# Optimization experiments

Measured on AMD Instinct MI355X. Metric: run time of the kernel, lower is better.

## Reference

```python
import jax, jax.numpy as jnp
import numpy as np
import math
from itertools import permutations

B, C_IN, C_OUT, K, N, D, F_DIM = 2, 4, 8, 4, 224, 2, 128


def _make_perms(k):
    # [k!, k, k] permutation matrices, same ordering as itertools.permutations
    nP = math.factorial(k)
    perms = np.zeros((nP, k, k), dtype=np.float32)
    for c, p in enumerate(permutations(range(k))):
        perms[c, np.arange(k), np.array(p)] = 1.0
    return jnp.asarray(perms)


def setup_inputs() -> dict:
    key = jax.random.key(0)
    ks = jax.random.split(key, 6)
    graph = jax.random.normal(ks[0], (B, C_IN, N, N), jnp.float32)
    types = jax.random.normal(ks[1], (B, C_IN, N), jnp.float32)
    features = jax.random.normal(ks[2], (B, N, F_DIM), jnp.float32)
    # xavier-uniform-ish scales for the learned kernels
    k_struct = jax.random.normal(ks[3], (C_OUT, C_IN, K, K), jnp.float32) * 0.3
    k_row = jax.random.normal(ks[4], (C_OUT, C_IN, K), jnp.float32) * 0.5
    k_col = jax.random.normal(ks[5], (C_OUT, C_IN, K), jnp.float32) * 0.5
    return {"graph": graph, "types": types, "features": features,
            "k_struct": k_struct, "k_row": k_row, "k_col": k_col}


def _forward(graph, types, features, k_struct, k_row, k_col):
    Bn, C, Nn, _ = graph.shape
    k = k_struct.shape[-1]
    new_k = (k - 1) * D + 1
    nH = Nn - new_k + 1            # square graph -> nW == nH
    n_sub = nH * nH
    idx = jnp.arange(nH)[:, None] + jnp.arange(k) * D  # [nH, k] dilated window indices

    # --- _prepare: dilated subgraph extraction (vectorized gather) ---
    g = graph[:, :, idx, :]            # [B,C,nH,k,N]
    g = g[..., idx]                    # [B,C,nH,k,nH,k]
    sub = jnp.transpose(g, (0, 2, 4, 1, 3, 5)).reshape(Bn, n_sub, C, k, k)
    rt = jnp.transpose(types[:, :, idx], (0, 2, 1, 3))  # [B,nH,C,k]
    row_t = jnp.broadcast_to(rt[:, :, None], (Bn, nH, nH, C, k)).reshape(Bn, n_sub, C, k)
    col_t = jnp.broadcast_to(rt[:, None, :], (Bn, nH, nH, C, k)).reshape(Bn, n_sub, C, k)
    rf = features[:, idx, :].sum(axis=-2)              # [B,nH,F]
    feats = rf[:, :, None, :] + rf[:, None, :, :]      # row_features + col_features
    h_mean = feats.reshape(Bn, n_sub, -1).mean(axis=1)  # [B,F]

    # --- permuted kernels ---
    perms = _make_perms(k)                                  # [P,k,k]
    Kp = jnp.einsum('pau,oiuv,pbv->oipab', perms, k_struct, perms)  # P K P^T
    Rp = jnp.einsum('pau,oiu->oipa', perms, k_row)
    Cp = jnp.einsum('pau,oiu->oipa', perms, k_col)

    subf = sub.reshape(-1, C, k, k)   # [n,i,a,b], n = B*n_sub
    rtf = row_t.reshape(-1, C, k)
    ctf = col_t.reshape(-1, C, k)

    # ||X - Y||_F^2 = ||X||^2 + ||Y||^2 - 2<X,Y>, avoids the huge broadcasted diff
    def sq_dist(x2_ni, y2_opi, cross_nopi):
        return y2_opi[None] + x2_ni[:, None, None, :] - 2.0 * cross_nopi

    G2 = jnp.sum(subf * subf, axis=(-2, -1))                       # [n,i]
    K2 = jnp.transpose(jnp.sum(Kp * Kp, axis=(-2, -1)), (0, 2, 1))  # [o,p,i]
    struct = sq_dist(G2, K2, jnp.einsum('niab,oipab->nopi', subf, Kp))
    R2 = jnp.transpose(jnp.sum(Rp * Rp, axis=-1), (0, 2, 1))
    rsim = sq_dist(jnp.sum(rtf * rtf, axis=-1), R2, jnp.einsum('nia,oipa->nopi', rtf, Rp))
    C2 = jnp.transpose(jnp.sum(Cp * Cp, axis=-1), (0, 2, 1))
    csim = sq_dist(jnp.sum(ctf * ctf, axis=-1), C2, jnp.einsum('nia,oipa->nopi', ctf, Cp))

    total = struct + rsim + csim            # [n, o, P, i]
    # maxpool over P of (-total), negated back == min over permutations of total
    pooled = jnp.min(total, axis=2)         # [n, o, i]
    sims = jnp.transpose(pooled.reshape(Bn, n_sub, -1), (0, 2, 1))  # [B, o*i, n_sub]
    out_sim = (1.0 - jax.nn.softmax(sims, axis=-1)) / sims.shape[-1]
    return h_mean, out_sim


def reference(graph, types, features, k_struct, k_row, k_col):
    return _forward(graph, types, features, k_struct, k_row, k_col)
```

## Files before the change

### kernel.cpp

```cpp
#include <hip/hip_runtime.h>
#include <hip/hip_bf16.h>

#define B_    2
#define CIN   4
#define COUT  8
#define KK    4
#define DD    2
#define NN    224
#define FDIM  128
#define NH    218
#define NSUB  (NH*NH)
#define NPERM 24
#define NROWS (B_*COUT*CIN)
#define NSUB4 (NSUB/4)
#define CH4   512
#define MB    ((NSUB4 + CH4 - 1) / CH4)
#define OG    2
#define NCH2  ((NSUB + 511) / 512)
#define NW    4
#define NPART (NCH2*NW)
#define NEGBIG (-3.4e38f)

typedef float v2f __attribute__((ext_vector_type(2)));

__device__ static constexpr int PERM[NPERM][4] = {
  {0,1,2,3},{0,1,3,2},{0,2,1,3},{0,2,3,1},{0,3,1,2},{0,3,2,1},
  {1,0,2,3},{1,0,3,2},{1,2,0,3},{1,2,3,0},{1,3,0,2},{1,3,2,0},
  {2,0,1,3},{2,0,3,1},{2,1,0,3},{2,1,3,0},{2,3,0,1},{2,3,1,0},
  {3,0,1,2},{3,0,2,1},{3,1,0,2},{3,1,2,0},{3,2,0,1},{3,2,1,0}
};

__global__ __launch_bounds__(64) void hmean_kernel(const float* __restrict__ features,
                                                   float* __restrict__ out) {
  int bf = blockIdx.x;
  int b = bf / FDIM, f = bf - b * FDIM;
  int lane = threadIdx.x;
  const float* fb = features + (size_t)b * NN * FDIM + f;
  float acc = 0.f;
  for (int r = lane; r < NN; r += 64) {
    int w = 0;
#pragma unroll
    for (int a = 0; a < KK; ++a) {
      int i0 = r - a * DD;
      if (0 <= i0 && i0 < NH) w++;
    }
    acc += (float)w * fb[(size_t)r * FDIM];
  }
#pragma unroll
  for (int off = 32; off > 0; off >>= 1) acc += __shfl_down(acc, off, 64);
  if (lane == 0) out[bf] = acc * (2.0f / (float)NH);
}

__global__ __launch_bounds__(256) void sims_kernel(
    const float* __restrict__ graph, const float* __restrict__ types,
    const float* __restrict__ ksA, const float* __restrict__ krA,
    const float* __restrict__ kcA, float* __restrict__ simsOut,
    float* __restrict__ partial)
{
  __shared__ float ls[COUT * CIN * 16];
  __shared__ float lr[COUT * CIN * 4];
  __shared__ float lc[COUT * CIN * 4];
  __shared__ float lK2[COUT * CIN];
  int t = threadIdx.x;
  for (int i = t; i < COUT * CIN * 16; i += 256) ls[i] = ksA[i];
  for (int i = t; i < COUT * CIN * 4; i += 256) { lr[i] = krA[i]; lc[i] = kcA[i]; }
  __syncthreads();
  if (t < COUT * CIN) {
    float k2 = 0.f;
#pragma unroll
    for (int u = 0; u < 16; ++u) k2 += ls[t * 16 + u] * ls[t * 16 + u];
#pragma unroll
    for (int u = 0; u < 4; ++u) k2 += lr[t * 4 + u] * lr[t * 4 + u] + lc[t * 4 + u] * lc[t * 4 + u];
    lK2[t] = k2;
  }
  __syncthreads();

  int s0r = blockIdx.x * 512 + t;
  int s1r = s0r + 256;
  bool v0 = (s0r < NSUB), v1 = (s1r < NSUB);
  int s0 = v0 ? s0r : (NSUB - 1);
  int s1 = v1 ? s1r : (NSUB - 1);
  int yi  = blockIdx.y;
  int og  = yi >> 3;
  int bci = yi & 7;
  int b   = bci >> 2;
  int ci  = bci & 3;
  int ii0 = s0 / NH, jj0 = s0 - ii0 * NH;
  int ii1 = s1 / NH, jj1 = s1 - ii1 * NH;

  const float* gi = graph + ((size_t)b * CIN + ci) * NN * NN;
  const float* ti = types + ((size_t)b * CIN + ci) * NN;

  v2f subv[16], rtv[4], ctv[4];
  v2f G2 = 0.f, T2r = 0.f, T2c = 0.f;
#pragma unroll
  for (int a = 0; a < KK; ++a) {
    const float* r0 = gi + (size_t)(ii0 + a * DD) * NN + jj0;
    const float* r1 = gi + (size_t)(ii1 + a * DD) * NN + jj1;
#pragma unroll
    for (int bb = 0; bb < KK; ++bb) {
      v2f v; v.x = r0[bb * DD]; v.y = r1[bb * DD];
      subv[a * 4 + bb] = v;
      G2 += v * v;
    }
    v2f rv; rv.x = ti[ii0 + a * DD]; rv.y = ti[ii1 + a * DD];
    v2f cv; cv.x = ti[jj0 + a * DD]; cv.y = ti[jj1 + a * DD];
    rtv[a] = rv; ctv[a] = cv;
    T2r += rv * rv; T2c += cv * cv;
  }
  v2f base0 = G2 + T2r + T2c;

  int wave = t >> 6, lane = t & 63;

#pragma unroll 1
  for (int oo = 0; oo < COUT / OG; ++oo) {
    int o = og * (COUT / OG) + oo;
    int oc = o * CIN + ci;
    float kS[16], kR[4], kC[4];
    {
      const float4* pS4 = (const float4*)(ls + oc * 16);
#pragma unroll
      for (int u = 0; u < 4; ++u) {
        float4 q = pS4[u];
        kS[u*4+0] = q.x; kS[u*4+1] = q.y; kS[u*4+2] = q.z; kS[u*4+3] = q.w;
      }
      float4 qr = *(const float4*)(lr + oc * 4);
      kR[0] = qr.x; kR[1] = qr.y; kR[2] = qr.z; kR[3] = qr.w;
      float4 qc = *(const float4*)(lc + oc * 4);
      kC[0] = qc.x; kC[1] = qc.y; kC[2] = qc.z; kC[3] = qc.w;
    }

    v2f C1[16];
#pragma unroll
    for (int a = 0; a < 4; ++a)
#pragma unroll
      for (int ap = 0; ap < 4; ++ap)
        C1[a * 4 + ap] = subv[a * 4 + a] * kS[ap * 4 + ap]
                       + rtv[a] * kR[ap] + ctv[a] * kC[ap];

    v2f pair01[16], pair23[16];
#pragma unroll
    for (int x = 0; x < 4; ++x)
#pragma unroll
      for (int y = 0; y < 4; ++y) {
        if (x == y) continue;
        pair01[x * 4 + y] = C1[0 * 4 + x] + C1[1 * 4 + y]
                          + subv[0*4+1] * kS[x*4+y] + subv[1*4+0] * kS[y*4+x];
        pair23[x * 4 + y] = C1[2 * 4 + x] + C1[3 * 4 + y]
                          + subv[2*4+3] * kS[x*4+y] + subv[3*4+2] * kS[y*4+x];
      }

    v2f maxcr = NEGBIG;
#pragma unroll
    for (int p = 0; p < NPERM; ++p) {
      const int p0 = PERM[p][0], p1 = PERM[p][1], p2 = PERM[p][2], p3 = PERM[p][3];
      v2f cr = pair01[p0 * 4 + p1] + pair23[p2 * 4 + p3];
      cr += subv[0*4+2] * kS[p0*4+p2];
      cr += subv[2*4+0] * kS[p2*4+p0];
      cr += subv[0*4+3] * kS[p0*4+p3];
      cr += subv[3*4+0] * kS[p3*4+p0];
      cr += subv[1*4+2] * kS[p1*4+p2];
      cr += subv[2*4+1] * kS[p2*4+p1];
      cr += subv[1*4+3] * kS[p1*4+p3];
      cr += subv[3*4+1] * kS[p3*4+p1];
      maxcr = __builtin_elementwise_max(maxcr, cr);
    }
    v2f best = base0 + lK2[oc] - 2.0f * maxcr;

    int rowIdx = (b * COUT + o) * CIN + ci;
    size_t rowbase = (size_t)rowIdx * NSUB;
    if (v0) simsOut[rowbase + s0r] = best.x;
    if (v1) simsOut[rowbase + s1r] = best.y;

    float bm0 = v0 ? best.x : NEGBIG;
    float bm1 = v1 ? best.y : NEGBIG;
    float m = fmaxf(bm0, bm1);
#pragma unroll
    for (int off = 32; off > 0; off >>= 1) m = fmaxf(m, __shfl_down(m, off, 64));
    m = __shfl(m, 0, 64);
    float e = 0.f;
    if (v0) e += __expf(bm0 - m);
    if (v1) e += __expf(bm1 - m);
#pragma unroll
    for (int off = 32; off > 0; off >>= 1) e += __shfl_down(e, off, 64);
    if (lane == 0) {
      int idx = ((rowIdx * NCH2 + blockIdx.x) * NW + wave) * 2;
      partial[idx] = m; partial[idx + 1] = e;
    }
  }
}

__global__ __launch_bounds__(256) void softmax_final(float* __restrict__ sims,
                                                     const float* __restrict__ partial) {
  int blk = blockIdx.x;
  int row = blk / MB;
  int ch  = blk - row * MB;
  int t = threadIdx.x;

  const float* pp = partial + (size_t)row * NPART * 2;
  float m = NEGBIG, l = 0.f;
  for (int i = t; i < NPART; i += 256) {
    float mi = pp[2 * i], li = pp[2 * i + 1];
    float M = fmaxf(m, mi);
    l = l * __expf(m - M) + li * __expf(mi - M);
    m = M;
  }
  __shared__ float ms[256], lsv[256];
  ms[t] = m; lsv[t] = l;
  __syncthreads();
  for (int off = 128; off > 0; off >>= 1) {
    if (t < off) {
      float m2 = ms[t + off], l2 = lsv[t + off];
      float M = fmaxf(ms[t], m2);
      lsv[t] = lsv[t] * __expf(ms[t] - M) + l2 * __expf(m2 - M);
      ms[t] = M;
    }
    __syncthreads();
  }
  float M = ms[0], invS = 1.0f / lsv[0];

  int base4 = ch * CH4;
  int n4 = NSUB4 - base4; if (n4 > CH4) n4 = CH4;
  float4* rp = (float4*)(sims + (size_t)row * NSUB) + base4;
  const float scale = 1.0f / (float)NSUB;
  for (int i = t; i < n4; i += 256) {
    float4 v = rp[i];
    v.x = (1.0f - __expf(v.x - M) * invS) * scale;
    v.y = (1.0f - __expf(v.y - M) * invS) * scale;
    v.z = (1.0f - __expf(v.z - M) * invS) * scale;
    v.w = (1.0f - __expf(v.w - M) * invS) * scale;
    rp[i] = v;
  }
}

extern "C" void kernel_launch(void* const* d_in, const int* in_sizes, int n_in,
                              void* d_out, int out_size, void* d_ws, size_t ws_size,
                              hipStream_t stream) {
  const float* graph    = (const float*)d_in[0];
  const float* types    = (const float*)d_in[1];
  const float* features = (const float*)d_in[2];
  const float* ks       = (const float*)d_in[3];
  const float* kr       = (const float*)d_in[4];
  const float* kc       = (const float*)d_in[5];
  float* out  = (float*)d_out;
  float* sims = out + B_ * FDIM;

  float* partial = (float*)d_ws;

  hmean_kernel<<<B_ * FDIM, 64, 0, stream>>>(features, out);
  dim3 sgrid(NCH2, B_ * CIN * OG);
  sims_kernel<<<sgrid, 256, 0, stream>>>(graph, types, ks, kr, kc, sims, partial);
  softmax_final<<<NROWS * MB, 256, 0, stream>>>(sims, partial);
}
```

Baseline: 103.7 us.

## Split softmax statistics into separate pass and add occupancy hint to sims kernel

Moves the per-wave max/exp-sum reductions out of the sims kernel into a new softmax_partial kernel that rereads sims in 2048-element chunks. softmax_final now merges only MB partials per row with a single-wave shuffle instead of a 256-thread shared-memory tree over many partials. The sims kernel also gets a launch_bounds occupancy hint of 4. The intent is to lighten the compute-heavy sims kernel and shrink the final merge, at the cost of an extra kernel launch and one more full read pass over the sims buffer.

New measurement: 100.8 us. 1.03x faster.

```diff
diff --git a/kernel.cpp b/kernel.cpp
--- a/kernel.cpp
+++ b/kernel.cpp
@@ -17,8 +17,6 @@
 #define MB    ((NSUB4 + CH4 - 1) / CH4)
 #define OG    2
 #define NCH2  ((NSUB + 511) / 512)
-#define NW    4
-#define NPART (NCH2*NW)
 #define NEGBIG (-3.4e38f)
 
 typedef float v2f __attribute__((ext_vector_type(2)));
@@ -51,11 +49,10 @@
   if (lane == 0) out[bf] = acc * (2.0f / (float)NH);
 }
 
-__global__ __launch_bounds__(256) void sims_kernel(
+__global__ __launch_bounds__(256, 4) void sims_kernel(
     const float* __restrict__ graph, const float* __restrict__ types,
     const float* __restrict__ ksA, const float* __restrict__ krA,
-    const float* __restrict__ kcA, float* __restrict__ simsOut,
-    float* __restrict__ partial)
+    const float* __restrict__ kcA, float* __restrict__ simsOut)
 {
   __shared__ float ls[COUT * CIN * 16];
   __shared__ float lr[COUT * CIN * 4];
@@ -110,8 +107,6 @@
   }
   v2f base0 = G2 + T2r + T2c;
 
-  int wave = t >> 6, lane = t & 63;
-
 #pragma unroll 1
   for (int oo = 0; oo < COUT / OG; ++oo) {
     int o = og * (COUT / OG) + oo;
@@ -167,57 +162,72 @@
     }
     v2f best = base0 + lK2[oc] - 2.0f * maxcr;
 
-    int rowIdx = (b * COUT + o) * CIN + ci;
-    size_t rowbase = (size_t)rowIdx * NSUB;
+    size_t rowbase = (size_t)((b * COUT + o) * CIN + ci) * NSUB;
     if (v0) simsOut[rowbase + s0r] = best.x;
     if (v1) simsOut[rowbase + s1r] = best.y;
-
-    float bm0 = v0 ? best.x : NEGBIG;
-    float bm1 = v1 ? best.y : NEGBIG;
-    float m = fmaxf(bm0, bm1);
-#pragma unroll
-    for (int off = 32; off > 0; off >>= 1) m = fmaxf(m, __shfl_down(m, off, 64));
-    m = __shfl(m, 0, 64);
-    float e = 0.f;
-    if (v0) e += __expf(bm0 - m);
-    if (v1) e += __expf(bm1 - m);
-#pragma unroll
-    for (int off = 32; off > 0; off >>= 1) e += __shfl_down(e, off, 64);
-    if (lane == 0) {
-      int idx = ((rowIdx * NCH2 + blockIdx.x) * NW + wave) * 2;
-      partial[idx] = m; partial[idx + 1] = e;
-    }
+  }
+}
+
+__global__ __launch_bounds__(256) void softmax_partial(const float* __restrict__ sims,
+                                                       float* __restrict__ partial) {
+  int ch = blockIdx.x, row = blockIdx.y;
+  int base4 = ch * CH4;
+  int n4 = NSUB4 - base4; if (n4 > CH4) n4 = CH4;
+  const float4* rp = (const float4*)(sims + (size_t)row * NSUB) + base4;
+  int t = threadIdx.x;
+  int wave = t >> 6, lane = t & 63;
+
+  float4 a0, a1;
+  bool h0 = (t < n4), h1 = (t + 256 < n4);
+  if (h0) a0 = rp[t];
+  if (h1) a1 = rp[t + 256];
+
+  float m = NEGBIG;
+  if (h0) m = fmaxf(fmaxf(a0.x, a0.y), fmaxf(a0.z, a0.w));
+  if (h1) m = fmaxf(m, fmaxf(fmaxf(a1.x, a1.y), fmaxf(a1.z, a1.w)));
+#pragma unroll
+  for (int off = 32; off > 0; off >>= 1) m = fmaxf(m, __shfl_down(m, off, 64));
+  __shared__ float red[8];
+  if (lane == 0) red[wave] = m;
+  __syncthreads();
+  float M = fmaxf(fmaxf(red[0], red[1]), fmaxf(red[2], red[3]));
+
+  float e = 0.f;
+  if (h0) e  = __expf(a0.x - M) + __expf(a0.y - M) + __expf(a0.z - M) + __expf(a0.w - M);
+  if (h1) e += __expf(a1.x - M) + __expf(a1.y - M) + __expf(a1.z - M) + __expf(a1.w - M);
+#pragma unroll
+  for (int off = 32; off > 0; off >>= 1) e += __shfl_down(e, off, 64);
+  if (lane == 0) red[4 + wave] = e;
+  __syncthreads();
+  if (t == 0) {
+    int idx = (row * MB + ch) * 2;
+    partial[idx] = M;
+    partial[idx + 1] = red[4] + red[5] + red[6] + red[7];
   }
 }
 
 __global__ __launch_bounds__(256) void softmax_final(float* __restrict__ sims,
                                                      const float* __restrict__ partial) {
-  int blk = blockIdx.x;
-  int row = blk / MB;
-  int ch  = blk - row * MB;
+  int ch = blockIdx.x, row = blockIdx.y;
   int t = threadIdx.x;
 
-  const float* pp = partial + (size_t)row * NPART * 2;
-  float m = NEGBIG, l = 0.f;
-  for (int i = t; i < NPART; i += 256) {
-    float mi = pp[2 * i], li = pp[2 * i + 1];
-    float M = fmaxf(m, mi);
-    l = l * __expf(m - M) + li * __expf(mi - M);
-    m = M;
-  }
-  __shared__ float ms[256], lsv[256];
-  ms[t] = m; lsv[t] = l;
-  __syncthreads();
-  for (int off = 128; off > 0; off >>= 1) {
-    if (t < off) {
-      float m2 = ms[t + off], l2 = lsv[t + off];
-      float M = fmaxf(ms[t], m2);
-      lsv[t] = lsv[t] * __expf(ms[t] - M) + l2 * __expf(m2 - M);
-      ms[t] = M;
-    }
-    __syncthreads();
-  }
-  float M = ms[0], invS = 1.0f / lsv[0];
+  __shared__ float sM, sInv;
+  if (t < 64) {
+    const float* pp = partial + row * MB * 2;
+    float m = NEGBIG, l = 0.f;
+    if (t < MB) { m = pp[2 * t]; l = pp[2 * t + 1]; }
+#pragma unroll
+    for (int off = 32; off > 0; off >>= 1) {
+      float m2 = __shfl_down(m, off, 64);
+      float l2 = __shfl_down(l, off, 64);
+      float M = fmaxf(m, m2);
+      l = l * __expf(m - M) + l2 * __expf(m2 - M);
+      m = M;
+    }
+    if (t == 0) { sM = m; sInv = 1.0f / l; }
+  }
+  __syncthreads();
+  float M = sM, invS = sInv;
 
   int base4 = ch * CH4;
   int n4 = NSUB4 - base4; if (n4 > CH4) n4 = CH4;
@@ -249,6 +259,8 @@
 
   hmean_kernel<<<B_ * FDIM, 64, 0, stream>>>(features, out);
   dim3 sgrid(NCH2, B_ * CIN * OG);
-  sims_kernel<<<sgrid, 256, 0, stream>>>(graph, types, ks, kr, kc, sims, partial);
-  softmax_final<<<NROWS * MB, 256, 0, stream>>>(sims, partial);
-}
+  sims_kernel<<<sgrid, 256, 0, stream>>>(graph, types, ks, kr, kc, sims);
+  dim3 pgrid(MB, NROWS);
+  softmax_partial<<<pgrid, 256, 0, stream>>>(sims, partial);
+  softmax_final<<<pgrid, 256, 0, stream>>>(sims, partial);
+}
```
